# Optimization experiments

Hardware: AMD Instinct MI355X
Metric: run time of the kernel (lower is better)

Reference implementation:

```python
import jax, jax.numpy as jnp
import numpy as np

NUM_TOKENS = 16384
MODEL_DIM = 4096
MAX_EXPERTS = 128
INITIAL_EXPERTS = 64
THRESHOLD = 0.5  # rm_threshold


def setup_inputs() -> dict:
    key = jax.random.key(0)
    k1, k2 = jax.random.split(key)
    x = jax.random.normal(k1, (NUM_TOKENS, MODEL_DIM), dtype=jnp.float32)
    # Linear(model_dim, max_expert_num, bias=False).weight -> [E_max, D]
    wg_weight = jax.random.normal(k2, (MAX_EXPERTS, MODEL_DIM), dtype=jnp.float32) * (1.0 / np.sqrt(MODEL_DIM))
    # experts_mask: first `INITIAL_EXPERTS` active
    experts_mask = (jnp.arange(MAX_EXPERTS) < INITIAL_EXPERTS).astype(jnp.float32)
    return {"x": x, "wg_weight": wg_weight, "experts_mask": experts_mask}


def reference(x, wg_weight, experts_mask):
    # gate logits: [N, E_max]
    scores = jnp.einsum("nd,ed->ne", x, wg_weight)
    # mask inactive experts
    scores = jnp.where(experts_mask[None, :] == 0, jnp.float32(-1e9), scores)
    # fp32 softmax + epsilon (matches F.softmax(..., dtype=float32) + 1e-14)
    scores = jax.nn.softmax(scores.astype(jnp.float32), axis=-1) + 1e-14
    # sort descending along expert dim
    sorted_scores = -jnp.sort(-scores, axis=-1)
    cum_scores = jnp.cumsum(sorted_scores, axis=-1)
    # adaptive top-k: experts needed to accumulate THRESHOLD routing mass
    mask = (cum_scores - sorted_scores) < THRESHOLD
    top_k = mask.sum(axis=-1).astype(jnp.int32)
    active_experts = experts_mask.sum().astype(jnp.int32)
    top_k = jnp.minimum(top_k, active_experts)
    return scores.astype(x.dtype), top_k
```

## Files before the change

kernel.cpp:

```cpp
#include <hip/hip_runtime.h>
#include <stdint.h>

#define NTOK 16384
#define DDIM 4096
#define NEXP 128
#define BM 16
#define BK 64
#define BKP 72

typedef __attribute__((ext_vector_type(8))) short short8;
typedef __attribute__((ext_vector_type(4))) float f32x4;

__device__ __forceinline__ uint32_t bf16_rne(float f) {
    uint32_t u = __float_as_uint(f);
    return (u + 0x7FFFu + ((u >> 16) & 1u)) >> 16;
}

__device__ __forceinline__ void split_bf16(float f, uint32_t& h, uint32_t& l) {
    h = bf16_rne(f);
    float r = f - __uint_as_float(h << 16);
    l = bf16_rne(r);
}

__device__ __forceinline__ void gld_lds16(const void* g, void* l) {
    __builtin_amdgcn_global_load_lds(
        (const __attribute__((address_space(1))) void*)g,
        (__attribute__((address_space(3))) void*)l, 16, 0, 0);
}

__global__ void prep_w(const float* __restrict__ w,
                       uint16_t* __restrict__ whi, uint16_t* __restrict__ wlo) {
    int i = (blockIdx.x * blockDim.x + threadIdx.x) * 4;
    float4 f = *(const float4*)(w + i);
    uint32_t h0, h1, h2, h3, l0, l1, l2, l3;
    split_bf16(f.x, h0, l0);
    split_bf16(f.y, h1, l1);
    split_bf16(f.z, h2, l2);
    split_bf16(f.w, h3, l3);
    *(uint2*)(whi + i) = make_uint2(h0 | (h1 << 16), h2 | (h3 << 16));
    *(uint2*)(wlo + i) = make_uint2(l0 | (l1 << 16), l2 | (l3 << 16));
}

__global__ __launch_bounds__(256, 4) void gate_gemm(
    const float* __restrict__ x,
    const uint16_t* __restrict__ whi, const uint16_t* __restrict__ wlo,
    float* __restrict__ S)
{
    __shared__ uint16_t sAh[BM * BKP], sAl[BM * BKP];
    __shared__ uint16_t sBh[NEXP * BK], sBl[NEXP * BK];

    const int tid  = threadIdx.x;
    const int lane = tid & 63;
    const int wave = tid >> 6;
    const int m0   = blockIdx.x * BM;
    const int q    = lane >> 4;
    const int c    = lane & 15;

    const int am  = tid >> 4;
    const int akc = tid & 15;
    const float* xp = x + (size_t)(m0 + am) * DDIM + akc * 4;

    float4 fa = *(const float4*)(xp);

    f32x4 acc[2];
    acc[0] = (f32x4){0.f, 0.f, 0.f, 0.f};
    acc[1] = (f32x4){0.f, 0.f, 0.f, 0.f};

    int bn[4], bkc[4];
    #pragma unroll
    for (int j = 0; j < 4; ++j) {
        const int p = (wave * 4 + j) * 64 + lane;
        bn[j]  = p >> 3;
        bkc[j] = (p & 7) ^ (bn[j] & 7);
    }

    for (int k0 = 0; k0 < DDIM; k0 += BK) {
        uint32_t h0, h1, h2, h3, l0, l1, l2, l3;
        split_bf16(fa.x, h0, l0);
        split_bf16(fa.y, h1, l1);
        split_bf16(fa.z, h2, l2);
        split_bf16(fa.w, h3, l3);
        *(uint2*)&sAh[am * BKP + akc * 4] = make_uint2(h0 | (h1 << 16), h2 | (h3 << 16));
        *(uint2*)&sAl[am * BKP + akc * 4] = make_uint2(l0 | (l1 << 16), l2 | (l3 << 16));

        #pragma unroll
        for (int j = 0; j < 4; ++j) {
            const size_t go = (size_t)bn[j] * DDIM + k0 + bkc[j] * 8;
            const int lb = (wave * 4 + j) * 512;
            gld_lds16(whi + go, sBh + lb);
            gld_lds16(wlo + go, sBl + lb);
        }
        __syncthreads();

        {
            const int kn = (k0 + BK < DDIM) ? (k0 + BK) : 0;
            fa = *(const float4*)(xp + kn);
        }

        #pragma unroll
        for (int ks = 0; ks < 2; ++ks) {
            const int kb  = ks * 32 + q * 8;
            const int kb8 = ks * 4 + q;
            short8 ah, al, bh[2], bl[2];
            {
                const int ro = c * BKP + kb;
                ah = *(const short8*)&sAh[ro];
                al = *(const short8*)&sAl[ro];
            }
            #pragma unroll
            for (int nt = 0; nt < 2; ++nt) {
                const int ne = wave * 32 + nt * 16 + c;
                const int ch = ne * 8 + (kb8 ^ (ne & 7));
                bh[nt] = *(const short8*)&sBh[ch * 8];
                bl[nt] = *(const short8*)&sBl[ch * 8];
            }
            #pragma unroll
            for (int nt = 0; nt < 2; ++nt) {
                acc[nt] = __builtin_amdgcn_mfma_f32_16x16x32_bf16(al, bh[nt], acc[nt], 0, 0, 0);
                acc[nt] = __builtin_amdgcn_mfma_f32_16x16x32_bf16(ah, bl[nt], acc[nt], 0, 0, 0);
                acc[nt] = __builtin_amdgcn_mfma_f32_16x16x32_bf16(ah, bh[nt], acc[nt], 0, 0, 0);
            }
        }
        __syncthreads();
    }

    #pragma unroll
    for (int nt = 0; nt < 2; ++nt) {
        const int e = wave * 32 + nt * 16 + c;
        #pragma unroll
        for (int r = 0; r < 4; ++r) {
            const int tok = m0 + q * 4 + r;
            S[(size_t)tok * NEXP + e] = acc[nt][r];
        }
    }
}

__global__ __launch_bounds__(256) void postproc(
    float* __restrict__ S, const float* __restrict__ mask,
    float* __restrict__ topk_out)
{
    const int lane = threadIdx.x & 63;
    const int wave = threadIdx.x >> 6;
    const int t = blockIdx.x * 4 + wave;
    float* row = S + (size_t)t * NEXP;

    float s0 = row[lane], s1 = row[lane + 64];
    float mk0 = mask[lane], mk1 = mask[lane + 64];
    const bool a0 = (mk0 != 0.f), a1 = (mk1 != 0.f);

    float mx = fmaxf(a0 ? s0 : -3.0e38f, a1 ? s1 : -3.0e38f);
    #pragma unroll
    for (int off = 32; off; off >>= 1) mx = fmaxf(mx, __shfl_xor(mx, off));

    float p0 = a0 ? __expf(s0 - mx) : 0.f;
    float p1 = a1 ? __expf(s1 - mx) : 0.f;
    float sum = p0 + p1;
    #pragma unroll
    for (int off = 32; off; off >>= 1) sum += __shfl_xor(sum, off);

    const float inv = 1.0f / sum;
    const float sc0 = p0 * inv + 1e-14f;
    const float sc1 = p1 * inv + 1e-14f;
    row[lane]      = sc0;
    row[lane + 64] = sc1;

    const int active = __popcll(__ballot(a0)) + __popcll(__ballot(a1));

    float v0 = sc0, v1 = sc1;
    float cum = 0.f;
    int k = 0;
    while (cum < 0.5f && k < NEXP) {
        float mv = fmaxf(v0, v1);
        #pragma unroll
        for (int off = 32; off; off >>= 1) mv = fmaxf(mv, __shfl_xor(mv, off));
        cum += mv;
        ++k;
        unsigned long long b = __ballot(v0 == mv || v1 == mv);
        int first = __ffsll(b) - 1;
        if (lane == first) {
            if (v0 == mv) v0 = -1.f; else v1 = -1.f;
        }
    }
    int topk = k < active ? k : active;
    if (lane == 0) topk_out[t] = (float)topk;
}

extern "C" void kernel_launch(void* const* d_in, const int* in_sizes, int n_in,
                              void* d_out, int out_size, void* d_ws, size_t ws_size,
                              hipStream_t stream) {
    (void)in_sizes; (void)n_in; (void)out_size; (void)ws_size;
    const float* x    = (const float*)d_in[0];
    const float* w    = (const float*)d_in[1];
    const float* mask = (const float*)d_in[2];

    float* S    = (float*)d_out;
    float* topk = S + (size_t)NTOK * NEXP;

    uint16_t* whi = (uint16_t*)d_ws;
    uint16_t* wlo = whi + (size_t)NEXP * DDIM;

    hipLaunchKernelGGL(prep_w, dim3((NEXP * DDIM) / (256 * 4)), dim3(256), 0, stream,
                       w, whi, wlo);
    hipLaunchKernelGGL(gate_gemm, dim3(NTOK / BM), dim3(256), 0, stream,
                       x, whi, wlo, S);
    hipLaunchKernelGGL(postproc, dim3(NTOK / 4), dim3(256), 0, stream,
                       S, mask, topk);
}
```

Before: 456.2 us.

## Enlarge gate GEMM token tile and split K across blocks

The token tile per block grows from 16 to 128 rows, with each wave computing a 64x64 sub-tile. Each weight tile loaded into LDS is now reused across many more tokens, which cuts redundant global and LDS traffic for the weights. To keep enough blocks in flight, K is split four ways into partial sums in workspace, and postproc adds them up before the softmax. This costs extra global writes and reads of four partial score matrices, more registers per thread, and lower occupancy.

```diff
diff --git a/kernel.cpp b/kernel.cpp
--- a/kernel.cpp
+++ b/kernel.cpp
@@ -4,12 +4,17 @@
 #define NTOK 16384
 #define DDIM 4096
 #define NEXP 128
-#define BM 16
+#define BM 128
 #define BK 64
+#define KSPLIT 4
+#define KSLICE (DDIM / KSPLIT)
+#define ITERS (KSLICE / BK)
 #define BKP 72
 
 typedef __attribute__((ext_vector_type(8))) short short8;
 typedef __attribute__((ext_vector_type(4))) float f32x4;
+
+union V16 { uint4 u; short8 s; };
 
 __device__ __forceinline__ uint32_t bf16_rne(float f) {
     uint32_t u = __float_as_uint(f);
@@ -20,6 +25,17 @@
     h = bf16_rne(f);
     float r = f - __uint_as_float(h << 16);
     l = bf16_rne(r);
+}
+
+__device__ __forceinline__ void split8(float4 f0, float4 f1, uint4& hi, uint4& lo) {
+    float a[8] = {f0.x, f0.y, f0.z, f0.w, f1.x, f1.y, f1.z, f1.w};
+    uint32_t h[8], l[8];
+    #pragma unroll
+    for (int j = 0; j < 8; ++j) split_bf16(a[j], h[j], l[j]);
+    hi = make_uint4(h[0] | (h[1] << 16), h[2] | (h[3] << 16),
+                    h[4] | (h[5] << 16), h[6] | (h[7] << 16));
+    lo = make_uint4(l[0] | (l[1] << 16), l[2] | (l[3] << 16),
+                    l[4] | (l[5] << 16), l[6] | (l[7] << 16));
 }
 
 __device__ __forceinline__ void gld_lds16(const void* g, void* l) {
@@ -41,10 +57,10 @@
     *(uint2*)(wlo + i) = make_uint2(l0 | (l1 << 16), l2 | (l3 << 16));
 }
 
-__global__ __launch_bounds__(256, 4) void gate_gemm(
+__global__ __launch_bounds__(256, 2) void gate_gemm(
     const float* __restrict__ x,
     const uint16_t* __restrict__ whi, const uint16_t* __restrict__ wlo,
-    float* __restrict__ S)
+    float* __restrict__ P)
 {
     __shared__ uint16_t sAh[BM * BKP], sAl[BM * BKP];
     __shared__ uint16_t sBh[NEXP * BK], sBl[NEXP * BK];
@@ -52,19 +68,22 @@
     const int tid  = threadIdx.x;
     const int lane = tid & 63;
     const int wave = tid >> 6;
-    const int m0   = blockIdx.x * BM;
-    const int q    = lane >> 4;
-    const int c    = lane & 15;
-
-    const int am  = tid >> 4;
-    const int akc = tid & 15;
-    const float* xp = x + (size_t)(m0 + am) * DDIM + akc * 4;
-
-    float4 fa = *(const float4*)(xp);
-
-    f32x4 acc[2];
-    acc[0] = (f32x4){0.f, 0.f, 0.f, 0.f};
-    acc[1] = (f32x4){0.f, 0.f, 0.f, 0.f};
+    const int mg   = blockIdx.x >> 2;
+    const int ksl  = blockIdx.x & 3;
+    const int m0   = mg * BM;
+    const int kbase = ksl * KSLICE;
+    const int q = lane >> 4;
+    const int c = lane & 15;
+    const int mw = wave >> 1;
+    const int nw = wave & 1;
+
+    const int arow  = tid >> 1;
+    const int ahalf = (tid & 1) * 32;
+    const float* xp = x + (size_t)(m0 + arow) * DDIM + kbase + ahalf;
+
+    float4 aP[8];
+    #pragma unroll
+    for (int j = 0; j < 8; ++j) aP[j] = *(const float4*)(xp + j * 4);
 
     int bn[4], bkc[4];
     #pragma unroll
@@ -74,18 +93,27 @@
         bkc[j] = (p & 7) ^ (bn[j] & 7);
     }
 
-    for (int k0 = 0; k0 < DDIM; k0 += BK) {
-        uint32_t h0, h1, h2, h3, l0, l1, l2, l3;
-        split_bf16(fa.x, h0, l0);
-        split_bf16(fa.y, h1, l1);
-        split_bf16(fa.z, h2, l2);
-        split_bf16(fa.w, h3, l3);
-        *(uint2*)&sAh[am * BKP + akc * 4] = make_uint2(h0 | (h1 << 16), h2 | (h3 << 16));
-        *(uint2*)&sAl[am * BKP + akc * 4] = make_uint2(l0 | (l1 << 16), l2 | (l3 << 16));
+    f32x4 acc[4][4];
+    #pragma unroll
+    for (int mt = 0; mt < 4; ++mt)
+        #pragma unroll
+        for (int nt = 0; nt < 4; ++nt)
+            acc[mt][nt] = (f32x4){0.f, 0.f, 0.f, 0.f};
+
+    for (int it = 0; it < ITERS; ++it) {
+        const int k0 = it * BK;
 
         #pragma unroll
         for (int j = 0; j < 4; ++j) {
-            const size_t go = (size_t)bn[j] * DDIM + k0 + bkc[j] * 8;
+            uint4 hi, lo;
+            split8(aP[2 * j], aP[2 * j + 1], hi, lo);
+            *(uint4*)&sAh[arow * BKP + ahalf + j * 8] = hi;
+            *(uint4*)&sAl[arow * BKP + ahalf + j * 8] = lo;
+        }
+
+        #pragma unroll
+        for (int j = 0; j < 4; ++j) {
+            const size_t go = (size_t)bn[j] * DDIM + kbase + k0 + bkc[j] * 8;
             const int lb = (wave * 4 + j) * 512;
             gld_lds16(whi + go, sBh + lb);
             gld_lds16(wlo + go, sBl + lb);
@@ -93,58 +121,69 @@
         __syncthreads();
 
         {
-            const int kn = (k0 + BK < DDIM) ? (k0 + BK) : 0;
-            fa = *(const float4*)(xp + kn);
+            const int kn = (it + 1 < ITERS) ? (k0 + BK) : 0;
+            #pragma unroll
+            for (int j = 0; j < 8; ++j) aP[j] = *(const float4*)(xp + kn + j * 4);
         }
 
         #pragma unroll
         for (int ks = 0; ks < 2; ++ks) {
             const int kb  = ks * 32 + q * 8;
             const int kb8 = ks * 4 + q;
-            short8 ah, al, bh[2], bl[2];
-            {
-                const int ro = c * BKP + kb;
-                ah = *(const short8*)&sAh[ro];
-                al = *(const short8*)&sAl[ro];
+            short8 ah[4], al[4];
+            #pragma unroll
+            for (int mt = 0; mt < 4; ++mt) {
+                const int ro = (mw * 64 + mt * 16 + c) * BKP + kb;
+                ah[mt] = *(const short8*)&sAh[ro];
+                al[mt] = *(const short8*)&sAl[ro];
             }
             #pragma unroll
-            for (int nt = 0; nt < 2; ++nt) {
-                const int ne = wave * 32 + nt * 16 + c;
+            for (int nt = 0; nt < 4; ++nt) {
+                const int ne = nw * 64 + nt * 16 + c;
                 const int ch = ne * 8 + (kb8 ^ (ne & 7));
-                bh[nt] = *(const short8*)&sBh[ch * 8];
-                bl[nt] = *(const short8*)&sBl[ch * 8];
+                short8 bh = *(const short8*)&sBh[ch * 8];
+                short8 bl = *(const short8*)&sBl[ch * 8];
+                #pragma unroll
+                for (int mt = 0; mt < 4; ++mt) {
+                    acc[mt][nt] = __builtin_amdgcn_mfma_f32_16x16x32_bf16(al[mt], bh, acc[mt][nt], 0, 0, 0);
+                    acc[mt][nt] = __builtin_amdgcn_mfma_f32_16x16x32_bf16(ah[mt], bl, acc[mt][nt], 0, 0, 0);
+                    acc[mt][nt] = __builtin_amdgcn_mfma_f32_16x16x32_bf16(ah[mt], bh, acc[mt][nt], 0, 0, 0);
+                }
             }
-            #pragma unroll
-            for (int nt = 0; nt < 2; ++nt) {
-                acc[nt] = __builtin_amdgcn_mfma_f32_16x16x32_bf16(al, bh[nt], acc[nt], 0, 0, 0);
-                acc[nt] = __builtin_amdgcn_mfma_f32_16x16x32_bf16(ah, bl[nt], acc[nt], 0, 0, 0);
-                acc[nt] = __builtin_amdgcn_mfma_f32_16x16x32_bf16(ah, bh[nt], acc[nt], 0, 0, 0);
+        }
+        __syncthreads();
+    }
+
+    float* Pp = P + (size_t)ksl * NTOK * NEXP;
+    #pragma unroll
+    for (int mt = 0; mt < 4; ++mt)
+        #pragma unroll
+        for (int nt = 0; nt < 4; ++nt) {
+            const int e = nw * 64 + nt * 16 + c;
+            #pragma unroll
+            for (int r = 0; r < 4; ++r) {
+                const int tok = m0 + mw * 64 + mt * 16 + q * 4 + r;
+                Pp[(size_t)tok * NEXP + e] = acc[mt][nt][r];
             }
         }
-        __syncthreads();
-    }
-
-    #pragma unroll
-    for (int nt = 0; nt < 2; ++nt) {
-        const int e = wave * 32 + nt * 16 + c;
-        #pragma unroll
-        for (int r = 0; r < 4; ++r) {
-            const int tok = m0 + q * 4 + r;
-            S[(size_t)tok * NEXP + e] = acc[nt][r];
-        }
-    }
 }
 
 __global__ __launch_bounds__(256) void postproc(
-    float* __restrict__ S, const float* __restrict__ mask,
-    float* __restrict__ topk_out)
+    const float* __restrict__ P, const float* __restrict__ mask,
+    float* __restrict__ S, float* __restrict__ topk_out)
 {
     const int lane = threadIdx.x & 63;
     const int wave = threadIdx.x >> 6;
     const int t = blockIdx.x * 4 + wave;
-    float* row = S + (size_t)t * NEXP;
-
-    float s0 = row[lane], s1 = row[lane + 64];
+
+    float s0 = 0.f, s1 = 0.f;
+    #pragma unroll
+    for (int ks = 0; ks < KSPLIT; ++ks) {
+        const float* row = P + ((size_t)ks * NTOK + t) * NEXP;
+        s0 += row[lane];
+        s1 += row[lane + 64];
+    }
+
     float mk0 = mask[lane], mk1 = mask[lane + 64];
     const bool a0 = (mk0 != 0.f), a1 = (mk1 != 0.f);
 
@@ -161,8 +200,9 @@
     const float inv = 1.0f / sum;
     const float sc0 = p0 * inv + 1e-14f;
     const float sc1 = p1 * inv + 1e-14f;
-    row[lane]      = sc0;
-    row[lane + 64] = sc1;
+    float* out = S + (size_t)t * NEXP;
+    out[lane]      = sc0;
+    out[lane + 64] = sc1;
 
     const int active = __popcll(__ballot(a0)) + __popcll(__ballot(a1));
 
@@ -198,11 +238,12 @@
 
     uint16_t* whi = (uint16_t*)d_ws;
     uint16_t* wlo = whi + (size_t)NEXP * DDIM;
+    float* P = (float*)(wlo + (size_t)NEXP * DDIM);
 
     hipLaunchKernelGGL(prep_w, dim3((NEXP * DDIM) / (256 * 4)), dim3(256), 0, stream,
                        w, whi, wlo);
-    hipLaunchKernelGGL(gate_gemm, dim3(NTOK / BM), dim3(256), 0, stream,
-                       x, whi, wlo, S);
+    hipLaunchKernelGGL(gate_gemm, dim3((NTOK / BM) * KSPLIT), dim3(256), 0, stream,
+                       x, whi, wlo, P);
     hipLaunchKernelGGL(postproc, dim3(NTOK / 4), dim3(256), 0, stream,
-                       S, mask, topk);
-}
+                       P, mask, S, topk);
+}
```

Result: faster. 418.8 us (-8.2%).
